# Kernel tuning notes

Measured on AMD Instinct MI355X. Metric: run time of the kernel, lower is better.

## Reference

```python
import jax, jax.numpy as jnp
import numpy as np

B, Q, NCLS1, C = 8, 900, 11, 256
NUM_ANCHOR = 100
H, W = 200, 200


def _make_view(b):
    # maps homogeneous (x0, y0, x1, y1, 1) box coords (meters-ish) to BEV pixels:
    # pixel = 20 * coord + 100  (keeps random boxes inside the 200x200 grid)
    v = np.zeros((5, 5), dtype=np.float32)
    for i in range(4):
        v[i, i] = 20.0
        v[i, 4] = 100.0
    v[4, 4] = 1.0
    return jnp.asarray(np.broadcast_to(v, (b, 5, 5)).copy())


def setup_inputs() -> dict:
    key = jax.random.key(0)
    k1, k2, k3 = jax.random.split(key, 3)
    return {
        "pred_boxes": jax.random.normal(k1, (B, Q, 4), dtype=jnp.float32),
        "pred_logits": jax.random.normal(k2, (B, Q, NCLS1), dtype=jnp.float32),
        "box_feats": jax.random.normal(k3, (B, Q, C), dtype=jnp.float32),
        "view": _make_view(B),
    }


def _box_to_bev(pred_boxes, pred_logits, box_feats, view):
    # scores = max over non-background classes of softmax(logits)
    scores = jnp.max(jax.nn.softmax(pred_logits, axis=-1)[..., :-1], axis=-1)  # [b,Q]
    _, idx = jax.lax.top_k(scores, NUM_ANCHOR)                                 # [b,N]

    boxes = jnp.take_along_axis(pred_boxes, idx[:, :, None], axis=1)[..., :4]  # [b,N,4]
    feats = jnp.take_along_axis(box_feats, idx[:, :, None], axis=1)            # [b,N,C]

    cx, cy = boxes[..., 0], boxes[..., 1]
    w, h = jnp.exp(boxes[..., 2]), jnp.exp(boxes[..., 3])
    xyxy = jnp.stack([cx - 0.5 * w, cy - 0.5 * h, cx + 0.5 * w, cy + 0.5 * h], axis=-1)
    xyxy1 = jnp.concatenate([xyxy, jnp.ones_like(xyxy[..., :1])], axis=-1)     # [b,N,5]

    coords = jnp.einsum("bij,bnj->bni", view, xyxy1)[..., :4].astype(jnp.int32)
    x0 = jnp.clip(coords[..., 0], 0, W)
    y0 = jnp.clip(coords[..., 1], 0, H)
    x1 = jnp.clip(coords[..., 2], 0, W)
    y1 = jnp.clip(coords[..., 3], 0, H)

    ys = jnp.arange(H, dtype=jnp.int32)
    xs = jnp.arange(W, dtype=jnp.int32)
    row = (ys[None, None, :] >= y0[:, :, None]) & (ys[None, None, :] < y1[:, :, None])  # [b,N,H]
    col = (xs[None, None, :] >= x0[:, :, None]) & (xs[None, None, :] < x1[:, :, None])  # [b,N,W]
    region = row[:, :, :, None] & col[:, :, None, :]                                    # [b,N,H,W]

    bev = jnp.einsum("bnhw,bnc->bhwc", region.astype(feats.dtype), feats)  # [b,H,W,C]
    mask = jnp.any(region, axis=1)                                          # [b,H,W]
    return bev, mask


def reference(pred_boxes, pred_logits, box_feats, view):
    return _box_to_bev(pred_boxes, pred_logits, box_feats, view)
```

## Files before the change

### kernel.cpp

```cpp
#include <hip/hip_runtime.h>
#include <math.h>

#define B_    8
#define Q_    900
#define NCLS_ 11
#define NANC_ 100
#define H_    200
#define W_    200
#define C_    256
#define HHALF 100
#define CHNK_ 113
#define CHEV_ 16
#define EVSTR_ 224

typedef float f32x4_ __attribute__((ext_vector_type(4)));

__global__ __launch_bounds__(128) void segdet_topk_kernel(
    const float* __restrict__ pred_boxes,
    const float* __restrict__ pred_logits,
    const float* __restrict__ view,
    int*  __restrict__ ws_idx,
    int4* __restrict__ ws_box)
{
    const int b     = blockIdx.x >> 3;
    const int chunk = blockIdx.x & 7;
    const int tid   = threadIdx.x;

    __shared__ __align__(16) float sc[Q_];

    for (int q2 = tid; q2 < Q_; q2 += 128) {
        const float* l = pred_logits + (b * Q_ + q2) * NCLS_;
        float v[NCLS_];
        float m = -INFINITY;
        #pragma unroll
        for (int i = 0; i < NCLS_; ++i) { v[i] = l[i]; m = fmaxf(m, v[i]); }
        float s = 0.0f, e10 = -INFINITY;
        #pragma unroll
        for (int i = 0; i < NCLS_; ++i) {
            float e = expf(v[i] - m);
            s += e;
            if (i < NCLS_ - 1) e10 = fmaxf(e10, e);
        }
        sc[q2] = e10 / s;
    }
    __syncthreads();

    const int q = chunk * CHNK_ + tid;
    if (tid < CHNK_ && q < Q_) {
        const float my = sc[q];
        int rank = 0;
        #pragma unroll 4
        for (int j4 = 0; j4 < Q_ / 4; ++j4) {
            const float4 o = *(const float4*)&sc[j4 * 4];
            const int j = j4 * 4;
            rank += (o.x > my) || (o.x == my && (j + 0) < q);
            rank += (o.y > my) || (o.y == my && (j + 1) < q);
            rank += (o.z > my) || (o.z == my && (j + 2) < q);
            rank += (o.w > my) || (o.w == my && (j + 3) < q);
        }
        if (rank < NANC_) {
            const float* bx = pred_boxes + (b * Q_ + q) * 4;
            double cx = (double)bx[0], cy = (double)bx[1];
            double w  = exp((double)bx[2]);
            double h  = exp((double)bx[3]);
            double p[5] = { cx - 0.5 * w, cy - 0.5 * h,
                            cx + 0.5 * w, cy + 0.5 * h, 1.0 };
            const float* v5 = view + b * 25;
            int ico[4];
            #pragma unroll
            for (int i = 0; i < 4; ++i) {
                double acc = 0.0;
                #pragma unroll
                for (int j = 0; j < 5; ++j) acc += (double)v5[i * 5 + j] * p[j];
                ico[i] = (int)acc;
            }
            int x0 = min(max(ico[0], 0), W_);
            int y0 = min(max(ico[1], 0), H_);
            int x1 = min(max(ico[2], 0), W_);
            int y1 = min(max(ico[3], 0), H_);
            const int slot = b * NANC_ + rank;
            ws_idx[slot] = q;
            ws_box[slot] = make_int4(x0, y0, x1, y1);
        }
    }
}

__device__ __forceinline__ void nt_store4(float* p, f32x4_ v) {
    __builtin_nontemporal_store(v, (f32x4_*)p);
}

__device__ __forceinline__ void gload_lds_16(const float* g, float* l) {
    __builtin_amdgcn_global_load_lds(
        (const __attribute__((address_space(1))) void*)g,
        (__attribute__((address_space(3))) void*)l,
        16, 0, 0);
}

__global__ __launch_bounds__(1024) void segdet_prep_kernel(
    const int*  __restrict__ ws_idx,
    const int4* __restrict__ ws_box,
    int*  __restrict__ g_hdr,
    int*  __restrict__ g_ev,
    float* __restrict__ mask)
{
    const int sub = threadIdx.x >> 8;
    const int t   = threadIdx.x & 255;
    const int ln  = threadIdx.x & 63;
    const int wv2 = (threadIdx.x >> 6) & 3;
    const int rid = blockIdx.x * 4 + sub;
    const int b   = rid / H_;
    const int h   = rid % H_;

    __shared__ __align__(16) int s_box[4][104];
    __shared__ int s_na[4];
    __shared__ int s_ws[4][4];

    if (wv2 == 0) {
        int na = 0;
        #pragma unroll
        for (int it = 0; it < 2; ++it) {
            int k = it * 64 + ln;
            bool act = false; int packed = 0;
            if (k < NANC_) {
                int4 bx = ws_box[b * NANC_ + k];
                int qi  = ws_idx[b * NANC_ + k];
                act = (bx.y <= h) && (h < bx.w) && (bx.x < bx.z);
                packed = bx.x | (bx.z << 8) | (qi << 16);
            }
            unsigned long long ball = __ballot(act);
            int pos = na + (int)__popcll(ball & ((1ull << ln) - 1ull));
            if (act) s_box[sub][pos] = packed;
            na += (int)__popcll(ball);
        }
        for (int idx = na + ln; idx < 104; idx += 64)
            s_box[sub][idx] = 0xFFFF;
        if (ln == 0) s_na[sub] = na;
    }
    __syncthreads();

    const int nact = s_na[sub];
    const int nk4  = (nact + 3) >> 2;

    int nopen = 0, ncl = 0, cov = 0;
#define CNT1_(PK) { const int x0_ = (PK) & 0xFF, x1_ = ((PK) >> 8) & 0xFF;    \
        nopen += (x0_ == t); ncl += (x1_ == t);                               \
        cov   += (x0_ <= t) && (t < x1_); }
    if (t < W_) {
        for (int k4 = 0; k4 < nk4; ++k4) {
            const int4 p4 = *(const int4*)&s_box[sub][k4 * 4];
            CNT1_(p4.x); CNT1_(p4.y); CNT1_(p4.z); CNT1_(p4.w);
        }
        mask[(size_t)rid * W_ + t] = (cov > 0) ? 1.0f : 0.0f;
    }
#undef CNT1_
    const int ntot = nopen + ncl;

    int incl = ntot;
    #pragma unroll
    for (int d = 1; d < 64; d <<= 1) {
        int u = __shfl_up(incl, d);
        incl = (ln >= d) ? incl + u : incl;
    }
    if (ln == 63) s_ws[sub][wv2] = incl;
    __syncthreads();

    int prev = 0;
    #pragma unroll
    for (int j = 0; j < 4; ++j) prev += (j < wv2) ? s_ws[sub][j] : 0;
    const int ne  = s_ws[sub][0] + s_ws[sub][1] + s_ws[sub][2] + s_ws[sub][3];
    const int ofs = prev + incl - ntot;
    if (t == 0) g_hdr[rid] = ne;

    if (t < W_ && ntot > 0) {
        int po = ofs, pc = ofs + nopen;
        int* dst = g_ev + (size_t)rid * EVSTR_;
#define SCT1_(PK) { const int x0_ = (PK) & 0xFF, x1_ = ((PK) >> 8) & 0xFF;    \
        const int q_ = (PK) >> 16;                                            \
        if (x0_ == t) dst[po++] = q_ | (t << 10);                             \
        if (x1_ == t) dst[pc++] = (int)((unsigned)q_ | ((unsigned)t << 10)    \
                                         | 0x80000000u); }
        for (int k4 = 0; k4 < nk4; ++k4) {
            const int4 p4 = *(const int4*)&s_box[sub][k4 * 4];
            SCT1_(p4.x); SCT1_(p4.y); SCT1_(p4.z); SCT1_(p4.w);
        }
#undef SCT1_
    }
}

__global__ __launch_bounds__(256) void segdet_bev2_kernel(
    const float* __restrict__ box_feats,
    const int*   __restrict__ g_hdr,
    const int*   __restrict__ g_ev,
    float* __restrict__ bev)
{
    const int hidx = blockIdx.x / B_;
    const int b    = blockIdx.x % B_;
    const int h    = (hidx & 1) ? (HHALF - 1 - (hidx >> 1)) : (HHALF + (hidx >> 1));
    const int rid  = b * H_ + h;

    const int tid = threadIdx.x;
    const int ln  = tid & 63;
    const int wv  = tid >> 6;

    __shared__ __align__(16) float s_chunk[2][CHEV_ * C_];
    __shared__ int s_e[EVSTR_];

    const int ne = g_hdr[rid];
    float* obase = bev + (size_t)rid * W_ * C_ + ln * 4;

    if (ne == 0) {
        const f32x4_ z = {0.f, 0.f, 0.f, 0.f};
        for (int w = wv; w < W_; w += 4)
            nt_store4(obase + (size_t)w * C_, z);
        return;
    }

    if (tid < EVSTR_) s_e[tid] = g_ev[(size_t)rid * EVSTR_ + tid];
    __syncthreads();

    const float* fbase = box_feats + (size_t)b * Q_ * C_ + ln * 4;
    const int nchunk = (ne + CHEV_ - 1) / CHEV_;

#define STAGE_(CI)                                                            \
    {                                                                         \
        const int base_ = (CI) * CHEV_;                                       \
        float* dst_ = &s_chunk[(CI) & 1][0];                                  \
        _Pragma("unroll")                                                     \
        for (int j = 0; j < 4; ++j) {                                         \
            const int e_ = base_ + wv * 4 + j;                                \
            if (e_ < ne) {                                                    \
                const int q_ = s_e[e_] & 0x3FF;                               \
                gload_lds_16(fbase + (size_t)q_ * C_,                         \
                             dst_ + (wv * 4 + j) * C_);                       \
            }                                                                 \
        }                                                                     \
    }

    STAGE_(0);
    __syncthreads();

    f32x4_ acc = {0.f, 0.f, 0.f, 0.f};
    int cnt = 0;
    int w = wv;
    for (int ci = 0; ci < nchunk; ++ci) {
        if (ci + 1 < nchunk) STAGE_(ci + 1);
        const int ebeg = ci * CHEV_;
        const int eend = (ne < ebeg + CHEV_) ? ne : (ebeg + CHEV_);
        const float* cb = &s_chunk[ci & 1][0];
        for (int e = ebeg; e < eend; ++e) {
            const int ent = s_e[e];
            const int pe  = (ent >> 10) & 0xFF;
            for (; w < pe; w += 4)
                nt_store4(obase + (size_t)w * C_, acc);
            const f32x4_ f = *(const f32x4_*)&cb[(e - ebeg) * C_ + ln * 4];
            if (ent < 0) { acc -= f; --cnt; }
            else         { acc += f; ++cnt; }
            if (cnt == 0) acc = (f32x4_){0.f, 0.f, 0.f, 0.f};
        }
        __syncthreads();
    }
#undef STAGE_
    for (; w < W_; w += 4)
        nt_store4(obase + (size_t)w * C_, acc);
}

__global__ __launch_bounds__(256) void segdet_bev_kernel(
    const float* __restrict__ box_feats,
    const int*   __restrict__ ws_idx,
    const int4*  __restrict__ ws_box,
    float* __restrict__ bev,
    float* __restrict__ mask)
{
    const int hidx = blockIdx.x / B_;
    const int b    = blockIdx.x % B_;
    const int h    = (hidx & 1) ? (HHALF - 1 - (hidx >> 1)) : (HHALF + (hidx >> 1));

    const int tid = threadIdx.x;
    const int ln  = tid & 63;
    const int wv  = tid >> 6;

    __shared__ __align__(16) float s_chunk[2][CHEV_ * C_];
    __shared__ int s_box[NANC_];
    __shared__ int s_nact;
    __shared__ int s_nopen[W_];
    __shared__ int s_ofs[W_ + 1];
    __shared__ int s_ent[2 * NANC_];
    __shared__ int s_wsum[4];

    if (tid < 64) {
        int na = 0;
        #pragma unroll
        for (int it = 0; it < 2; ++it) {
            int k = it * 64 + ln;
            bool act = false;
            int packed = 0;
            if (k < NANC_) {
                int4 bx = ws_box[b * NANC_ + k];
                int qi  = ws_idx[b * NANC_ + k];
                act = (bx.y <= h) && (h < bx.w) && (bx.x < bx.z);
                packed = bx.x | (bx.z << 8) | (qi << 16);
            }
            unsigned long long ball = __ballot(act);
            int pos = na + (int)__popcll(ball & ((1ull << ln) - 1ull));
            if (act) s_box[pos] = packed;
            na += (int)__popcll(ball);
        }
        if (ln == 0) s_nact = na;
    }
    __syncthreads();

    const int nact = s_nact;
    float* obase = bev + (size_t)(b * H_ + h) * W_ * C_ + ln * 4;
    float* mrow  = mask + (size_t)(b * H_ + h) * W_;

    if (nact == 0) {
        const f32x4_ z = {0.f, 0.f, 0.f, 0.f};
        for (int w = wv; w < W_; w += 4)
            nt_store4(obase + (size_t)w * C_, z);
        if (tid < W_) __builtin_nontemporal_store(0.0f, &mrow[tid]);
        return;
    }

    int ntot = 0;
    if (tid < W_) {
        int nopen = 0, nclose = 0, cov = 0;
        for (int k = 0; k < nact; ++k) {
            int pk = s_box[k];
            int x0 = pk & 0xFF, x1 = (pk >> 8) & 0xFF;
            nopen  += (x0 == tid);
            nclose += (x1 == tid);
            cov    += (x0 <= tid) && (tid < x1);
        }
        s_nopen[tid] = nopen;
        ntot = nopen + nclose;
        __builtin_nontemporal_store((cov > 0) ? 1.0f : 0.0f, &mrow[tid]);
    }

    int incl = ntot;
    #pragma unroll
    for (int d = 1; d < 64; d <<= 1) {
        int u = __shfl_up(incl, d);
        incl = (ln >= d) ? incl + u : incl;
    }
    if (ln == 63) s_wsum[wv] = incl;
    __syncthreads();

    int prev = 0;
    #pragma unroll
    for (int j = 0; j < 4; ++j) prev += (j < wv) ? s_wsum[j] : 0;
    const int ne = s_wsum[0] + s_wsum[1] + s_wsum[2] + s_wsum[3];
    if (tid < W_) s_ofs[tid] = prev + incl - ntot;
    if (tid == 0) s_ofs[W_] = ne;
    __syncthreads();

    if (tid < nact) {
        int pk = s_box[tid];
        int x0 = pk & 0xFF, x1 = (pk >> 8) & 0xFF, q = pk >> 16;
        int ro = 0, rc = 0;
        for (int j = 0; j < tid; ++j) {
            int pj = s_box[j];
            ro += ((pj & 0xFF) == x0);
            rc += (((pj >> 8) & 0xFF) == x1);
        }
        s_ent[s_ofs[x0] + ro] = q | (x0 << 10);
        if (x1 < W_)
            s_ent[s_ofs[x1] + s_nopen[x1] + rc] =
                (int)((unsigned)q | ((unsigned)x1 << 10) | 0x80000000u);
    }
    __syncthreads();

    const float* fbase = box_feats + (size_t)b * Q_ * C_ + ln * 4;
    const int nchunk = (ne + CHEV_ - 1) / CHEV_;

#define STAGE_(CI)                                                            \
    {                                                                         \
        const int base_ = (CI) * CHEV_;                                       \
        float* dst_ = &s_chunk[(CI) & 1][0];                                  \
        _Pragma("unroll")                                                     \
        for (int j = 0; j < 4; ++j) {                                         \
            const int e_ = base_ + wv * 4 + j;                                \
            if (e_ < ne) {                                                    \
                const int q_ = s_ent[e_] & 0x3FF;                             \
                gload_lds_16(fbase + (size_t)q_ * C_,                         \
                             dst_ + (wv * 4 + j) * C_);                       \
            }                                                                 \
        }                                                                     \
    }

    STAGE_(0);
    __syncthreads();

    f32x4_ acc = {0.f, 0.f, 0.f, 0.f};
    int cnt = 0;
    int w = wv;
    for (int ci = 0; ci < nchunk; ++ci) {
        if (ci + 1 < nchunk) STAGE_(ci + 1);
        const int ebeg = ci * CHEV_;
        const int eend = (ne < ebeg + CHEV_) ? ne : (ebeg + CHEV_);
        const float* cb = &s_chunk[ci & 1][0];
        for (int e = ebeg; e < eend; ++e) {
            const int ent = s_ent[e];
            const int pe  = (ent >> 10) & 0xFF;
            for (; w < pe; w += 4)
                nt_store4(obase + (size_t)w * C_, acc);
            const f32x4_ f = *(const f32x4_*)&cb[(e - ebeg) * C_ + ln * 4];
            if (ent < 0) { acc -= f; --cnt; }
            else         { acc += f; ++cnt; }
            if (cnt == 0) acc = (f32x4_){0.f, 0.f, 0.f, 0.f};
        }
        __syncthreads();
    }
#undef STAGE_
    for (; w < W_; w += 4)
        nt_store4(obase + (size_t)w * C_, acc);
}

extern "C" void kernel_launch(void* const* d_in, const int* in_sizes, int n_in,
                              void* d_out, int out_size, void* d_ws, size_t ws_size,
                              hipStream_t stream) {
    const float* pred_boxes  = (const float*)d_in[0];
    const float* pred_logits = (const float*)d_in[1];
    const float* box_feats   = (const float*)d_in[2];
    const float* view        = (const float*)d_in[3];

    float* bev  = (float*)d_out;
    float* mask = bev + (size_t)B_ * H_ * W_ * C_;

    int*  ws_idx = (int*)d_ws;
    int4* ws_box = (int4*)((char*)d_ws + 3200);
    int*  g_hdr  = (int*)((char*)d_ws + 16000);
    int*  g_ev   = (int*)((char*)d_ws + 22400);
    const size_t need = 22400ull + (size_t)B_ * H_ * EVSTR_ * 4ull;

    segdet_topk_kernel<<<B_ * 8, 128, 0, stream>>>(pred_boxes, pred_logits, view,
                                                   ws_idx, ws_box);
    if (ws_size >= need) {
        segdet_prep_kernel<<<(B_ * H_) / 4, 1024, 0, stream>>>(
            ws_idx, ws_box, g_hdr, g_ev, mask);
        segdet_bev2_kernel<<<B_ * H_, 256, 0, stream>>>(
            box_feats, g_hdr, g_ev, bev);
    } else {
        segdet_bev_kernel<<<B_ * H_, 256, 0, stream>>>(
            box_feats, ws_idx, ws_box, bev, mask);
    }
}
```

Measured before the change: 113.7 us.

## Split each BEV row into two column halves with precomputed midpoint accumulator

The prep kernel now also computes, for each row, the sum of features of boxes spanning the column midpoint along with their count. It records event offsets so the events can be split at the midpoint. The bev2 kernel launches twice as many blocks, each handling half a row and seeding the right half with the midpoint accumulator, which doubles parallelism for the write-bound sweep. In exchange the prep kernel does extra global feature gathers per row, and the workspace requirement grows.

Result: slower. 118.6 us (+4.4%).

```diff
diff --git a/kernel.cpp b/kernel.cpp
--- a/kernel.cpp
+++ b/kernel.cpp
@@ -97,10 +97,12 @@
 }
 
 __global__ __launch_bounds__(1024) void segdet_prep_kernel(
-    const int*  __restrict__ ws_idx,
-    const int4* __restrict__ ws_box,
-    int*  __restrict__ g_hdr,
-    int*  __restrict__ g_ev,
+    const float* __restrict__ box_feats,
+    const int*   __restrict__ ws_idx,
+    const int4*  __restrict__ ws_box,
+    int*   __restrict__ g_hdr,
+    int*   __restrict__ g_ev,
+    float* __restrict__ acc_mid,
     float* __restrict__ mask)
 {
     const int sub = threadIdx.x >> 8;
@@ -169,7 +171,6 @@
     for (int j = 0; j < 4; ++j) prev += (j < wv2) ? s_ws[sub][j] : 0;
     const int ne  = s_ws[sub][0] + s_ws[sub][1] + s_ws[sub][2] + s_ws[sub][3];
     const int ofs = prev + incl - ntot;
-    if (t == 0) g_hdr[rid] = ne;
 
     if (t < W_ && ntot > 0) {
         int po = ofs, pc = ofs + nopen;
@@ -185,16 +186,36 @@
         }
 #undef SCT1_
     }
+
+    float accm = 0.0f;
+    int cm = 0;
+    for (int k4 = 0; k4 < nk4; ++k4) {
+        const int4 p4 = *(const int4*)&s_box[sub][k4 * 4];
+#define MID1_(PK) { const int x0_ = (PK) & 0xFF, x1_ = ((PK) >> 8) & 0xFF;    \
+        if (x0_ <= HHALF && HHALF < x1_) {                                    \
+            accm += box_feats[((size_t)b * Q_ + ((PK) >> 16)) * C_ + t];      \
+            ++cm; } }
+        MID1_(p4.x); MID1_(p4.y); MID1_(p4.z); MID1_(p4.w);
+#undef MID1_
+    }
+    acc_mid[(size_t)rid * C_ + t] = accm;
+
+    if (t == 0)   { g_hdr[rid * 4 + 0] = ne; g_hdr[rid * 4 + 3] = cm; }
+    if (t == 100) { g_hdr[rid * 4 + 1] = ofs;
+                    g_hdr[rid * 4 + 2] = ofs + ntot; }
 }
 
 __global__ __launch_bounds__(256) void segdet_bev2_kernel(
     const float* __restrict__ box_feats,
     const int*   __restrict__ g_hdr,
     const int*   __restrict__ g_ev,
+    const float* __restrict__ acc_mid,
     float* __restrict__ bev)
 {
-    const int hidx = blockIdx.x / B_;
-    const int b    = blockIdx.x % B_;
+    const int bb   = blockIdx.x >> 1;
+    const int seg  = blockIdx.x & 1;
+    const int hidx = bb / B_;
+    const int b    = bb % B_;
     const int h    = (hidx & 1) ? (HHALF - 1 - (hidx >> 1)) : (HHALF + (hidx >> 1));
     const int rid  = b * H_ + h;
 
@@ -205,21 +226,27 @@
     __shared__ __align__(16) float s_chunk[2][CHEV_ * C_];
     __shared__ int s_e[EVSTR_];
 
-    const int ne = g_hdr[rid];
+    const int4 hd = *(const int4*)&g_hdr[rid * 4];
+    const int evbase = seg ? hd.z : 0;
+    const int evcnt  = seg ? (hd.x - hd.z) : hd.y;
+    const int segb   = seg * HHALF;
+
     float* obase = bev + (size_t)rid * W_ * C_ + ln * 4;
 
-    if (ne == 0) {
-        const f32x4_ z = {0.f, 0.f, 0.f, 0.f};
-        for (int w = wv; w < W_; w += 4)
-            nt_store4(obase + (size_t)w * C_, z);
-        return;
-    }
-
-    if (tid < EVSTR_) s_e[tid] = g_ev[(size_t)rid * EVSTR_ + tid];
-    __syncthreads();
+    f32x4_ acc = {0.f, 0.f, 0.f, 0.f};
+    int cnt = 0;
+    if (seg) {
+        acc = *(const f32x4_*)&acc_mid[(size_t)rid * C_ + ln * 4];
+        cnt = hd.w;
+    }
+
+    if (evcnt > 0) {
+        if (tid < evcnt) s_e[tid] = g_ev[(size_t)rid * EVSTR_ + evbase + tid];
+        __syncthreads();
+    }
 
     const float* fbase = box_feats + (size_t)b * Q_ * C_ + ln * 4;
-    const int nchunk = (ne + CHEV_ - 1) / CHEV_;
+    const int nchunk = (evcnt + CHEV_ - 1) / CHEV_;
 
 #define STAGE_(CI)                                                            \
     {                                                                         \
@@ -228,7 +255,7 @@
         _Pragma("unroll")                                                     \
         for (int j = 0; j < 4; ++j) {                                         \
             const int e_ = base_ + wv * 4 + j;                                \
-            if (e_ < ne) {                                                    \
+            if (e_ < evcnt) {                                                 \
                 const int q_ = s_e[e_] & 0x3FF;                               \
                 gload_lds_16(fbase + (size_t)q_ * C_,                         \
                              dst_ + (wv * 4 + j) * C_);                       \
@@ -236,31 +263,33 @@
         }                                                                     \
     }
 
-    STAGE_(0);
-    __syncthreads();
-
-    f32x4_ acc = {0.f, 0.f, 0.f, 0.f};
-    int cnt = 0;
-    int w = wv;
-    for (int ci = 0; ci < nchunk; ++ci) {
-        if (ci + 1 < nchunk) STAGE_(ci + 1);
-        const int ebeg = ci * CHEV_;
-        const int eend = (ne < ebeg + CHEV_) ? ne : (ebeg + CHEV_);
-        const float* cb = &s_chunk[ci & 1][0];
-        for (int e = ebeg; e < eend; ++e) {
-            const int ent = s_e[e];
-            const int pe  = (ent >> 10) & 0xFF;
-            for (; w < pe; w += 4)
-                nt_store4(obase + (size_t)w * C_, acc);
-            const f32x4_ f = *(const f32x4_*)&cb[(e - ebeg) * C_ + ln * 4];
-            if (ent < 0) { acc -= f; --cnt; }
-            else         { acc += f; ++cnt; }
-            if (cnt == 0) acc = (f32x4_){0.f, 0.f, 0.f, 0.f};
-        }
+    int w = segb + wv;
+    const int wend = segb + HHALF;
+    if (nchunk > 0) {
+        STAGE_(0);
         __syncthreads();
+        for (int ci = 0; ci < nchunk; ++ci) {
+            if (ci + 1 < nchunk) STAGE_(ci + 1);
+            const int ebeg = ci * CHEV_;
+            const int eend = (evcnt < ebeg + CHEV_) ? evcnt : (ebeg + CHEV_);
+            const float* cb = &s_chunk[ci & 1][0];
+            for (int e = ebeg; e < eend; ++e) {
+                const int ent = s_e[e];
+                const int pe  = (ent >> 10) & 0xFF;
+                for (; w < pe; w += 4)
+                    nt_store4(obase + (size_t)w * C_, acc);
+                const f32x4_ f = *(const f32x4_*)&cb[(e - ebeg) * C_ + ln * 4];
+                if (ent < 0) { acc -= f; --cnt; }
+                else         { acc += f; ++cnt; }
+                if (cnt == 0) acc = (f32x4_){0.f, 0.f, 0.f, 0.f};
+            }
+            __syncthreads();
+        }
+    } else if (cnt == 0) {
+        acc = (f32x4_){0.f, 0.f, 0.f, 0.f};
     }
 #undef STAGE_
-    for (; w < W_; w += 4)
+    for (; w < wend; w += 4)
         nt_store4(obase + (size_t)w * C_, acc);
 }
 
@@ -426,19 +455,20 @@
     float* bev  = (float*)d_out;
     float* mask = bev + (size_t)B_ * H_ * W_ * C_;
 
-    int*  ws_idx = (int*)d_ws;
-    int4* ws_box = (int4*)((char*)d_ws + 3200);
-    int*  g_hdr  = (int*)((char*)d_ws + 16000);
-    int*  g_ev   = (int*)((char*)d_ws + 22400);
-    const size_t need = 22400ull + (size_t)B_ * H_ * EVSTR_ * 4ull;
+    int*   ws_idx  = (int*)d_ws;
+    int4*  ws_box  = (int4*)((char*)d_ws + 3200);
+    int*   g_hdr   = (int*)((char*)d_ws + 16000);
+    int*   g_ev    = (int*)((char*)d_ws + 41600);
+    float* acc_mid = (float*)((char*)d_ws + 1475200);
+    const size_t need = 1475200ull + 1638400ull;
 
     segdet_topk_kernel<<<B_ * 8, 128, 0, stream>>>(pred_boxes, pred_logits, view,
                                                    ws_idx, ws_box);
     if (ws_size >= need) {
         segdet_prep_kernel<<<(B_ * H_) / 4, 1024, 0, stream>>>(
-            ws_idx, ws_box, g_hdr, g_ev, mask);
-        segdet_bev2_kernel<<<B_ * H_, 256, 0, stream>>>(
-            box_feats, g_hdr, g_ev, bev);
+            box_feats, ws_idx, ws_box, g_hdr, g_ev, acc_mid, mask);
+        segdet_bev2_kernel<<<B_ * H_ * 2, 256, 0, stream>>>(
+            box_feats, g_hdr, g_ev, acc_mid, bev);
     } else {
         segdet_bev_kernel<<<B_ * H_, 256, 0, stream>>>(
             box_feats, ws_idx, ws_box, bev, mask);
```
